# Optimization experiments

Measured on AMD Instinct MI355X. Metric: run time of the kernel, lower is better.

The kernel has to match this reference:

```python
import jax, jax.numpy as jnp
import numpy as np

N, E, G = 100000, 400000, 64
IN, H, C = 8, 4, 64
HD = H * C  # 256


def setup_inputs() -> dict:
    key = jax.random.key(0)
    ks = jax.random.split(key, 40)
    f = lambda k, shp, s=0.05: jax.random.normal(k, shp, jnp.float32) * s
    inp = {
        "x": jax.random.normal(ks[0], (N, IN), jnp.float32),
        "edge_attr": jax.random.normal(ks[1], (E, 1), jnp.float32),
        "src": jax.random.randint(ks[2], (E,), 0, N),
        "dst": jax.random.randint(ks[3], (E,), 0, N),
        "batch": jnp.sort(jax.random.randint(ks[4], (N,), 0, G)),
        # encoder Linear(8 -> 64)
        "W_enc": f(ks[5], (IN, C)), "b_enc": jnp.zeros((C,), jnp.float32),
        # GATv2 layer 1: in 64 -> H*C=256
        "g1_Wl": f(ks[6], (C, HD)), "g1_bl": jnp.zeros((HD,), jnp.float32),
        "g1_Wr": f(ks[7], (C, HD)), "g1_br": jnp.zeros((HD,), jnp.float32),
        "g1_We": f(ks[8], (1, HD)),
        "g1_att": f(ks[9], (H, C)),
        "g1_bias": jnp.zeros((HD,), jnp.float32),
        # GATv2 layer 2: in 256 -> 256
        "g2_Wl": f(ks[10], (HD, HD)), "g2_bl": jnp.zeros((HD,), jnp.float32),
        "g2_Wr": f(ks[11], (HD, HD)), "g2_br": jnp.zeros((HD,), jnp.float32),
        "g2_We": f(ks[12], (1, HD)),
        "g2_att": f(ks[13], (H, C)),
        "g2_bias": jnp.zeros((HD,), jnp.float32),
        # post MLP: 256 -> 128 -> LN -> relu -> 128 -> 64 -> relu, head 64 -> 1
        "W_p1": f(ks[14], (HD, 128)), "b_p1": jnp.zeros((128,), jnp.float32),
        "ln_g": jnp.ones((128,), jnp.float32), "ln_b": jnp.zeros((128,), jnp.float32),
        "W_p2": f(ks[15], (128, 64)), "b_p2": jnp.zeros((64,), jnp.float32),
        "W_head": f(ks[16], (64, 1)), "b_head": jnp.zeros((1,), jnp.float32),
    }
    return inp


def gatv2(x, src, dst, e_attr, Wl, bl, Wr, br, We, att, bias):
    """PyG GATv2Conv: score = att . LeakyReLU(xl[src] + xr[dst] + e), scatter-softmax over dst,
    out_i = sum_j alpha_ij * xl[j], concat heads, + bias."""
    n = x.shape[0]
    xl = (x @ Wl + bl).reshape(n, H, C)          # source-side transform
    xr = (x @ Wr + br).reshape(n, H, C)          # target-side transform
    ee = (e_attr @ We).reshape(-1, H, C)         # [E,H,C]
    s = jax.nn.leaky_relu(xl[src] + xr[dst] + ee, 0.2)
    logit = jnp.einsum('ehc,hc->eh', s, att)     # [E,H]
    # numerically-stable scatter softmax over edges sharing a target node
    m = jax.ops.segment_max(logit, dst, num_segments=n)
    m = jnp.where(jnp.isfinite(m), m, 0.0)
    ex = jnp.exp(logit - m[dst])
    den = jax.ops.segment_sum(ex, dst, num_segments=n)
    alpha = ex / (den[dst] + 1e-16)
    out = jax.ops.segment_sum(alpha[:, :, None] * xl[src], dst, num_segments=n)
    return out.reshape(n, HD) + bias


def reference(x, edge_attr, src, dst, batch,
              W_enc, b_enc,
              g1_Wl, g1_bl, g1_Wr, g1_br, g1_We, g1_att, g1_bias,
              g2_Wl, g2_bl, g2_Wr, g2_br, g2_We, g2_att, g2_bias,
              W_p1, b_p1, ln_g, ln_b, W_p2, b_p2, W_head, b_head):
    h = jax.nn.relu(x @ W_enc + b_enc)
    h = jax.nn.relu(gatv2(h, src, dst, edge_attr, g1_Wl, g1_bl, g1_Wr, g1_br, g1_We, g1_att, g1_bias))
    h = jax.nn.relu(gatv2(h, src, dst, edge_attr, g2_Wl, g2_bl, g2_Wr, g2_br, g2_We, g2_att, g2_bias))
    # global mean pool per graph
    sums = jax.ops.segment_sum(h, batch, num_segments=G)
    cnt = jax.ops.segment_sum(jnp.ones((h.shape[0],), h.dtype), batch, num_segments=G)
    p = sums / jnp.maximum(cnt, 1.0)[:, None]
    # post MLP (dropout is identity at inference)
    p = p @ W_p1 + b_p1
    mu = jnp.mean(p, axis=-1, keepdims=True)
    var = jnp.mean((p - mu) ** 2, axis=-1, keepdims=True)
    p = (p - mu) * jax.lax.rsqrt(var + 1e-5) * ln_g + ln_b
    p = jax.nn.relu(p)
    p = jax.nn.relu(p @ W_p2 + b_p2)
    return (p @ W_head + b_head)[:, 0]  # [G]
```

## Files before the change

### kernel.cpp

```cpp
#include <hip/hip_runtime.h>
#include <hip/hip_fp16.h>
#include <math.h>


#define HD 256
#define NHEAD 4
#define CH 64

typedef _Float16 half8 __attribute__((ext_vector_type(8)));
typedef _Float16 h2 __attribute__((ext_vector_type(2)));
typedef __attribute__((ext_vector_type(4))) float f32x4;

__device__ __forceinline__ h2 pack_h2(float a, float b) {
#if __has_builtin(__builtin_amdgcn_cvt_pkrtz)
    return __builtin_bit_cast(h2, __builtin_amdgcn_cvt_pkrtz(a, b));
#else
    return h2{(_Float16)a, (_Float16)b};
#endif
}

__device__ __forceinline__ void prep_one(const float* Wl, const float* Wr,
                                         ushort* frag, int K, int t) {
    int l = t & 63;
    int ct = (t >> 6) & 31;
    int ks = t >> 11;
    int n = l & 15, q = l >> 4;
    const float* W = (ct < 16) ? Wl : Wr;
    int col = (ct & 15) * 16 + n;
    ushort* phi = frag + (size_t)t * 8;
#pragma unroll
    for (int j = 0; j < 8; ++j) {
        int k = ks * 32 + q * 8 + j;
        float wv = W[(size_t)k * 256 + col];
        phi[j] = __half_as_ushort(__float2half(wv));
    }
}

__global__ void setup_kernel(int* __restrict__ zbase, int nzero,
                             const float* __restrict__ Wl1, const float* __restrict__ Wr1,
                             ushort* __restrict__ f1,
                             const float* __restrict__ Wl2, const float* __restrict__ Wr2,
                             ushort* __restrict__ f2) {
    int i = blockIdx.x * 256 + threadIdx.x;
    if (i < nzero) {
        zbase[i] = 0;
    } else {
        int gt = i - nzero;
        if (gt < 64 * 64) prep_one(Wl1, Wr1, f1, 64, gt);
        else if (gt < 64 * 64 + 256 * 64) prep_one(Wl2, Wr2, f2, 256, gt - 64 * 64);
    }
}

__global__ void deg_kernel(const int* __restrict__ dst, int* __restrict__ cnt, int E) {
    int e = blockIdx.x * 256 + threadIdx.x;
    if (e < E) atomicAdd(&cnt[dst[e]], 1);
}

__global__ void scan_block(const int* __restrict__ cnt, int* __restrict__ off,
                           int* __restrict__ bsum, int N) {
    __shared__ int s[256];
    int i = blockIdx.x * 256 + threadIdx.x;
    int v = (i < N) ? cnt[i] : 0;
    s[threadIdx.x] = v;
    __syncthreads();
    for (int d = 1; d < 256; d <<= 1) {
        int t = 0;
        if (threadIdx.x >= d) t = s[threadIdx.x - d];
        __syncthreads();
        s[threadIdx.x] += t;
        __syncthreads();
    }
    if (i < N) off[i + 1] = s[threadIdx.x];
    if (threadIdx.x == 255) bsum[blockIdx.x] = s[255];
    if (blockIdx.x == 0 && threadIdx.x == 0) off[0] = 0;
}

__global__ void scan_add2(int* __restrict__ off, const int* __restrict__ bsum, int N) {
    __shared__ int red[4];
    int b = blockIdx.x;
    int s = 0;
    for (int i = threadIdx.x; i < b; i += 256) s += bsum[i];
    for (int o = 32; o > 0; o >>= 1) s += __shfl_xor(s, o);
    if ((threadIdx.x & 63) == 0) red[threadIdx.x >> 6] = s;
    __syncthreads();
    int prefix = red[0] + red[1] + red[2] + red[3];
    int i = b * 256 + threadIdx.x;
    if (i < N) off[i + 1] += prefix;
}

__global__ void scatter_kernel(const int* __restrict__ dst, const int* __restrict__ src,
                               const float* __restrict__ eattr, const int* __restrict__ off,
                               int* __restrict__ cur, int2* __restrict__ edata, int E) {
    int e = blockIdx.x * 256 + threadIdx.x;
    if (e < E) {
        int d = dst[e];
        int p = atomicAdd(&cur[d], 1);
        edata[off[d] + p] = make_int2(src[e], __float_as_int(eattr[e]));
    }
}

template <int K, bool FUSE_ENC>
__global__ __launch_bounds__(512, 4) void gemm_mfma(
    const void* Av, const float* __restrict__ Wenc, const float* __restrict__ benc,
    const ushort* __restrict__ Bfrag,
    const float* __restrict__ bl, const float* __restrict__ br,
    ushort* __restrict__ outL, ushort* outR, int N) {
    constexpr int KS = K / 32;
    constexpr int C4 = K / 4;
    constexpr int LC4 = (K == 256) ? 6 : 4;
    constexpr int FRAG_SHORTS = KS * 4 * 64 * 8;
    constexpr int TB_STRIDE = 260;
    constexpr int SH_BYTES = (FRAG_SHORTS * 2 > 64 * TB_STRIDE * 2)
                                 ? FRAG_SHORTS * 2 : 64 * TB_STRIDE * 2;
    __shared__ __align__(16) char shraw[SH_BYTES];
    ushort* frag = (ushort*)shraw;
    ushort* tbuf = (ushort*)shraw;

    const int t = threadIdx.x;
    const int row0 = blockIdx.x * 64;
    const float* Ax = (const float*)Av;
    const ushort* Ahalf = (const ushort*)Av;

#pragma unroll
    for (int it = 0; it < (64 * C4) / 512; ++it) {
        int jj = it * 512 + t;
        int m = jj & 15;
        int c4 = (jj >> 4) & (C4 - 1);
        int rg = jj >> (4 + LC4);
        int row = row0 + rg * 16 + m;
        ushort4 sv = make_ushort4(0, 0, 0, 0);
        if constexpr (FUSE_ENC) {
            if (row < N) {
                float4 xa = *(const float4*)(Ax + (size_t)row * 8);
                float4 xb = *(const float4*)(Ax + (size_t)row * 8 + 4);
                float xrv[8] = {xa.x, xa.y, xa.z, xa.w, xb.x, xb.y, xb.z, xb.w};
                ushort o[4];
#pragma unroll
                for (int j = 0; j < 4; ++j) {
                    int c = c4 * 4 + j;
                    float a = benc[c];
#pragma unroll
                    for (int u = 0; u < 8; ++u) a = fmaf(xrv[u], Wenc[u * 64 + c], a);
                    o[j] = __half_as_ushort(__float2half(fmaxf(a, 0.f)));
                }
                sv = make_ushort4(o[0], o[1], o[2], o[3]);
            }
        } else {
            if (row < N) sv = *(const ushort4*)(Ahalf + (size_t)row * K + c4 * 4);
        }
        int c = c4 * 4;
        int ks = c >> 5, q = (c >> 3) & 3, jb = c & 7;
        int cell = (ks * 4 + rg) * 64 + m + 16 * q;
        *(ushort4*)(frag + cell * 8 + jb) = sv;
    }
    __syncthreads();

    const int w = t >> 6, l = t & 63;
    const int ct0 = w * 4;

    f32x4 acc[4][4];
#pragma unroll
    for (int rt = 0; rt < 4; ++rt)
#pragma unroll
        for (int c = 0; c < 4; ++c) acc[rt][c] = (f32x4){0.f, 0.f, 0.f, 0.f};

#pragma unroll
    for (int ks = 0; ks < KS; ++ks) {
        half8 a[4];
#pragma unroll
        for (int rt = 0; rt < 4; ++rt) {
            int cell = (ks * 4 + rt) * 64 + l;
            a[rt] = *(const half8*)(frag + cell * 8);
        }
#pragma unroll
        for (int c = 0; c < 4; ++c) {
            size_t e = ((size_t)(ks * 32 + ct0 + c) * 64 + l) * 8;
            half8 bh = *(const half8*)(Bfrag + e);
#pragma unroll
            for (int rt = 0; rt < 4; ++rt)
                acc[rt][c] = __builtin_amdgcn_mfma_f32_16x16x32_f16(a[rt], bh, acc[rt][c], 0, 0, 0);
        }
    }

    const int m = l & 15, q = l >> 4;
#pragma unroll
    for (int half = 0; half < 2; ++half) {
        __syncthreads();
        if ((w >> 2) == half) {
            const float* bias = half ? br : bl;
#pragma unroll
            for (int c = 0; c < 4; ++c) {
                int col = ((ct0 + c) & 15) * 16 + m;
                float bb = bias[col];
#pragma unroll
                for (int rt = 0; rt < 4; ++rt)
#pragma unroll
                    for (int r = 0; r < 4; ++r)
                        tbuf[(rt * 16 + q * 4 + r) * TB_STRIDE + col] =
                            __half_as_ushort(__float2half(acc[rt][c][r] + bb));
            }
        }
        __syncthreads();
        ushort* outp = half ? outR : outL;
#pragma unroll
        for (int it = 0; it < 4; ++it) {
            int jj = it * 512 + t;
            int row = jj >> 5;
            int ch = jj & 31;
            int grow = row0 + row;
            if (grow < N) {
                uint2 a0 = *(const uint2*)(tbuf + row * TB_STRIDE + ch * 8);
                uint2 a1 = *(const uint2*)(tbuf + row * TB_STRIDE + ch * 8 + 4);
                *(uint4*)(outp + (size_t)grow * 256 + ch * 8) =
                    make_uint4(a0.x, a0.y, a1.x, a1.y);
            }
        }
    }
}

__global__ __launch_bounds__(256) void gat_aggregate(
    const ushort* __restrict__ xl, const ushort* xr,
    const int* __restrict__ off, const int2* __restrict__ edata,
    const float* __restrict__ We, const float* __restrict__ att,
    const float* __restrict__ bias, ushort* out, int N) {
    int node = blockIdx.x * 4 + (threadIdx.x >> 6);
    if (node >= N) return;
    int lane = threadIdx.x & 63;
    int cbase = (lane >> 4) * 64 + (lane & 15) * 4;

    float4 wef = *(const float4*)(We + cbase);
    float4 atf = *(const float4*)(att + cbase);
    h2 we_lo = {(_Float16)wef.x, (_Float16)wef.y};
    h2 we_hi = {(_Float16)wef.z, (_Float16)wef.w};
    h2 at_lo = {(_Float16)atf.x, (_Float16)atf.y};
    h2 at_hi = {(_Float16)atf.z, (_Float16)atf.w};
    size_t nb = (size_t)node * HD;
    uint2 xru = *(const uint2*)(xr + nb + cbase);
    h2 xr_lo = __builtin_bit_cast(h2, xru.x);
    h2 xr_hi = __builtin_bit_cast(h2, xru.y);
    float4 b4 = *(const float4*)(bias + cbase);
    const h2 c02 = {(_Float16)0.2f, (_Float16)0.2f};
    const h2 z2 = {(_Float16)0.f, (_Float16)0.f};

    float l = 0.f;
    h2 acc_lo = z2, acc_hi = z2;

    int s0i = off[node], s1i = off[node + 1];
    int j[4];
    float ea[4];
#pragma unroll
    for (int u = 0; u < 4; ++u) {
        int tt = s0i + u;
        int2 ed = (tt < s1i) ? edata[tt] : make_int2(0, 0);
        j[u] = ed.x;
        ea[u] = __int_as_float(ed.y);
    }
    for (int t = s0i; t < s1i; t += 4) {
        int nE = s1i - t;
        if (nE > 4) nE = 4;
        int jc[4];
        float eac[4];
#pragma unroll
        for (int u = 0; u < 4; ++u) { jc[u] = j[u]; eac[u] = ea[u]; }
        h2 xlo[4], xhi[4];
#pragma unroll
        for (int u = 0; u < 4; ++u) {
            xlo[u] = z2; xhi[u] = z2;
            if (u < nE) {
                uint2 xu = *(const uint2*)(xl + (size_t)jc[u] * HD + cbase);
                xlo[u] = __builtin_bit_cast(h2, xu.x);
                xhi[u] = __builtin_bit_cast(h2, xu.y);
            }
        }
        if (t + 4 < s1i) {
#pragma unroll
            for (int u = 0; u < 4; ++u) {
                int tt = t + 4 + u;
                int2 ed = (tt < s1i) ? edata[tt] : make_int2(0, 0);
                j[u] = ed.x;
                ea[u] = __int_as_float(ed.y);
            }
        }
        float rr[4];
#pragma unroll
        for (int u = 0; u < 4; ++u) {
            _Float16 eh = (_Float16)eac[u];
            h2 e2 = {eh, eh};
            h2 s0 = e2 * we_lo + (xlo[u] + xr_lo);
            h2 s1 = e2 * we_hi + (xhi[u] + xr_hi);
            s0 = __builtin_elementwise_max(s0, z2) + __builtin_elementwise_min(s0, z2) * c02;
            s1 = __builtin_elementwise_max(s1, z2) + __builtin_elementwise_min(s1, z2) * c02;
            float v;
#if __has_builtin(__builtin_amdgcn_fdot2)
            v = __builtin_amdgcn_fdot2(__builtin_bit_cast(__fp16 __attribute__((ext_vector_type(2))), at_lo),
                                       __builtin_bit_cast(__fp16 __attribute__((ext_vector_type(2))), s0),
                                       0.f, false);
            v = __builtin_amdgcn_fdot2(__builtin_bit_cast(__fp16 __attribute__((ext_vector_type(2))), at_hi),
                                       __builtin_bit_cast(__fp16 __attribute__((ext_vector_type(2))), s1),
                                       v, false);
#else
            v = (float)at_lo.x * (float)s0.x + (float)at_lo.y * (float)s0.y
              + (float)at_hi.x * (float)s1.x + (float)at_hi.y * (float)s1.y;
#endif
            rr[u] = v;
        }
        h2 r01 = pack_h2(rr[0], rr[1]);
        h2 r23 = pack_h2(rr[2], rr[3]);
#pragma unroll
        for (int o = 1; o <= 8; o <<= 1) {
            int v01 = __shfl_xor(__builtin_bit_cast(int, r01), o);
            int v23 = __shfl_xor(__builtin_bit_cast(int, r23), o);
            r01 = r01 + __builtin_bit_cast(h2, v01);
            r23 = r23 + __builtin_bit_cast(h2, v23);
        }
        float r0 = (float)r01.x, r1 = (float)r01.y;
        float r2 = (float)r23.x, r3 = (float)r23.y;
        if (1 >= nE) r1 = -1e30f;
        if (2 >= nE) r2 = -1e30f;
        if (3 >= nE) r3 = -1e30f;
        float p0 = __expf(r0);
        float p1 = __expf(r1);
        float p2 = __expf(r2);
        float p3 = __expf(r3);
        l += (p0 + p1) + (p2 + p3);
        h2 ph0 = pack_h2(p0, p0);
        h2 ph1 = pack_h2(p1, p1);
        h2 ph2 = pack_h2(p2, p2);
        h2 ph3 = pack_h2(p3, p3);
        acc_lo = ph0 * xlo[0] + acc_lo;
        acc_hi = ph0 * xhi[0] + acc_hi;
        acc_lo = ph1 * xlo[1] + acc_lo;
        acc_hi = ph1 * xhi[1] + acc_hi;
        acc_lo = ph2 * xlo[2] + acc_lo;
        acc_hi = ph2 * xhi[2] + acc_hi;
        acc_lo = ph3 * xlo[3] + acc_lo;
        acc_hi = ph3 * xhi[3] + acc_hi;
    }
    float inv = 1.f / (l + 1e-16f);
    float ax = (float)acc_lo.x, ay = (float)acc_lo.y;
    float az = (float)acc_hi.x, aw = (float)acc_hi.y;
    ushort4 o;
    o.x = __half_as_ushort(__float2half(fmaxf(fmaf(ax, inv, b4.x), 0.f)));
    o.y = __half_as_ushort(__float2half(fmaxf(fmaf(ay, inv, b4.y), 0.f)));
    o.z = __half_as_ushort(__float2half(fmaxf(fmaf(az, inv, b4.z), 0.f)));
    o.w = __half_as_ushort(__float2half(fmaxf(fmaf(aw, inv, b4.w), 0.f)));
    *(ushort4*)(out + nb + cbase) = o;
}

__device__ __forceinline__ int lowerb(const int* b, int n, int v) {
    int lo = 0, hi = n;
    while (lo < hi) {
        int mid = (lo + hi) >> 1;
        if (b[mid] < v) lo = mid + 1; else hi = mid;
    }
    return lo;
}

__global__ void pool_kernel(const ushort* __restrict__ h, const int* __restrict__ batch,
                            float* __restrict__ pooled, float* __restrict__ gcnt, int N) {
    int g = blockIdx.x >> 3, part = blockIdx.x & 7;
    int start = lowerb(batch, N, g);
    int end = lowerb(batch, N, g + 1);
    int rows = end - start;
    int r0 = start + (int)((long long)rows * part / 8);
    int r1 = start + (int)((long long)rows * (part + 1) / 8);
    int c = threadIdx.x;
    float s = 0.f;
    for (int r = r0; r < r1; ++r)
        s += __half2float(__ushort_as_half(h[(size_t)r * HD + c]));
    atomicAdd(&pooled[g * HD + c], s);
    if (part == 0 && c == 0) gcnt[g] = (float)rows;
}

__global__ void mlp_kernel(const float* __restrict__ pooled, const float* __restrict__ gcnt,
                           const float* __restrict__ W_p1, const float* __restrict__ b_p1,
                           const float* __restrict__ ln_g, const float* __restrict__ ln_b,
                           const float* __restrict__ W_p2, const float* __restrict__ b_p2,
                           const float* __restrict__ W_head, const float* __restrict__ b_head,
                           float* __restrict__ out) {
    int g = blockIdx.x;
    int j = threadIdx.x;
    __shared__ float sh[128];
    __shared__ float red[2];

    float inv = 1.f / fmaxf(gcnt[g], 1.f);
    float v = b_p1[j];
    for (int k = 0; k < 256; ++k) v = fmaf(pooled[g * 256 + k] * inv, W_p1[k * 128 + j], v);

    float s = v;
    for (int o = 32; o > 0; o >>= 1) s += __shfl_xor(s, o);
    if ((j & 63) == 0) red[j >> 6] = s;
    __syncthreads();
    float mu = (red[0] + red[1]) * (1.f / 128.f);
    float d = v - mu;
    float s2 = d * d;
    for (int o = 32; o > 0; o >>= 1) s2 += __shfl_xor(s2, o);
    __syncthreads();
    if ((j & 63) == 0) red[j >> 6] = s2;
    __syncthreads();
    float var = (red[0] + red[1]) * (1.f / 128.f);

    float p = d * rsqrtf(var + 1e-5f) * ln_g[j] + ln_b[j];
    sh[j] = fmaxf(p, 0.f);
    __syncthreads();

    if (j < 64) {
        float q = b_p2[j];
        for (int k = 0; k < 128; ++k) q = fmaf(sh[k], W_p2[k * 64 + j], q);
        q = fmaxf(q, 0.f);
        float t = q * W_head[j];
        for (int o = 32; o > 0; o >>= 1) t += __shfl_xor(t, o);
        if (j == 0) out[g] = t + b_head[0];
    }
}

extern "C" void kernel_launch(void* const* d_in, const int* in_sizes, int n_in,
                              void* d_out, int out_size, void* d_ws, size_t ws_size,
                              hipStream_t stream) {
    const float* x      = (const float*)d_in[0];
    const float* eattr  = (const float*)d_in[1];
    const int*   src    = (const int*)d_in[2];
    const int*   dst    = (const int*)d_in[3];
    const int*   batch  = (const int*)d_in[4];
    const float* W_enc  = (const float*)d_in[5];
    const float* b_enc  = (const float*)d_in[6];
    const float* g1_Wl  = (const float*)d_in[7];
    const float* g1_bl  = (const float*)d_in[8];
    const float* g1_Wr  = (const float*)d_in[9];
    const float* g1_br  = (const float*)d_in[10];
    const float* g1_We  = (const float*)d_in[11];
    const float* g1_att = (const float*)d_in[12];
    const float* g1_bias= (const float*)d_in[13];
    const float* g2_Wl  = (const float*)d_in[14];
    const float* g2_bl  = (const float*)d_in[15];
    const float* g2_Wr  = (const float*)d_in[16];
    const float* g2_br  = (const float*)d_in[17];
    const float* g2_We  = (const float*)d_in[18];
    const float* g2_att = (const float*)d_in[19];
    const float* g2_bias= (const float*)d_in[20];
    const float* W_p1   = (const float*)d_in[21];
    const float* b_p1   = (const float*)d_in[22];
    const float* ln_g   = (const float*)d_in[23];
    const float* ln_b   = (const float*)d_in[24];
    const float* W_p2   = (const float*)d_in[25];
    const float* b_p2   = (const float*)d_in[26];
    const float* W_head = (const float*)d_in[27];
    const float* b_head = (const float*)d_in[28];

    const int N = in_sizes[0] / 8;
    const int E = in_sizes[2];

    char* p = (char*)d_ws;
    auto alloc = [&](size_t bytes) -> void* {
        void* r = (void*)p;
        p += (bytes + 255) & ~(size_t)255;
        return r;
    };
    ushort* bufA   = (ushort*)alloc((size_t)N * HD * 2);
    ushort* bufXL  = (ushort*)alloc((size_t)N * HD * 2);
    int*    cnt    = (int*)alloc((size_t)N * 4);
    int*    curp   = (int*)alloc((size_t)N * 4);
    float*  pooled = (float*)alloc(64 * HD * 4);
    char*   zend   = p;
    int*    off    = (int*)alloc((size_t)(N + 1) * 4);
    int2*   edata  = (int2*)alloc((size_t)E * 8);
    const int nb   = (N + 255) / 256;
    int*    bsum   = (int*)alloc((size_t)nb * 4);
    float*  gcnt   = (float*)alloc(64 * 4);
    ushort* wfrag1 = (ushort*)alloc((size_t)64 * 64 * 16 * 2);
    ushort* wfrag2 = (ushort*)alloc((size_t)256 * 64 * 16 * 2);

    const int nzero = (int)(((char*)zend - (char*)cnt) / 4);
    const int nsetup = nzero + 64 * 64 + 256 * 64;

    setup_kernel<<<(nsetup + 255) / 256, 256, 0, stream>>>(
        cnt, nzero, g1_Wl, g1_Wr, wfrag1, g2_Wl, g2_Wr, wfrag2);

    deg_kernel<<<(E + 255) / 256, 256, 0, stream>>>(dst, cnt, E);
    scan_block<<<nb, 256, 0, stream>>>(cnt, off, bsum, N);
    scan_add2<<<nb, 256, 0, stream>>>(off, bsum, N);
    scatter_kernel<<<(E + 255) / 256, 256, 0, stream>>>(dst, src, eattr, off, curp,
                                                        edata, E);

    const int gblocks = (N + 63) / 64;
    const int ablocks = (N + 3) / 4;

    gemm_mfma<64, true><<<gblocks, 512, 0, stream>>>(
        x, W_enc, b_enc, wfrag1, g1_bl, g1_br, bufXL, bufA, N);
    gat_aggregate<<<ablocks, 256, 0, stream>>>(
        bufXL, bufA, off, edata, g1_We, g1_att, g1_bias, bufA, N);

    gemm_mfma<256, false><<<gblocks, 512, 0, stream>>>(
        bufA, nullptr, nullptr, wfrag2, g2_bl, g2_br, bufXL, bufA, N);
    gat_aggregate<<<ablocks, 256, 0, stream>>>(
        bufXL, bufA, off, edata, g2_We, g2_att, g2_bias, bufA, N);

    pool_kernel<<<64 * 8, 256, 0, stream>>>(bufA, batch, pooled, gcnt, N);
    mlp_kernel<<<64, 128, 0, stream>>>(pooled, gcnt, W_p1, b_p1, ln_g, ln_b,
                                       W_p2, b_p2, W_head, b_head, (float*)d_out);
}
```

Baseline: 438.6 us.

## Process two nodes per wavefront in GAT aggregation with 16-byte gathers

```diff
diff --git a/kernel.cpp b/kernel.cpp
--- a/kernel.cpp
+++ b/kernel.cpp
@@ -16,6 +16,16 @@
     return __builtin_bit_cast(h2, __builtin_amdgcn_cvt_pkrtz(a, b));
 #else
     return h2{(_Float16)a, (_Float16)b};
+#endif
+}
+
+__device__ __forceinline__ float dot2f(h2 a, h2 b, float c) {
+#if __has_builtin(__builtin_amdgcn_fdot2)
+    typedef __fp16 fp16v2 __attribute__((ext_vector_type(2)));
+    return __builtin_amdgcn_fdot2(__builtin_bit_cast(fp16v2, a),
+                                  __builtin_bit_cast(fp16v2, b), c, false);
+#else
+    return c + (float)a.x * (float)b.x + (float)a.y * (float)b.y;
 #endif
 }
 
@@ -95,7 +105,7 @@
     if (e < E) {
         int d = dst[e];
         int p = atomicAdd(&cur[d], 1);
-        edata[off[d] + p] = make_int2(src[e], __float_as_int(eattr[e]));
+        edata[off[d] + p] = make_int2(src[e] << 9, __float_as_int(eattr[e]));
     }
 }
 
@@ -223,29 +233,45 @@
     const int* __restrict__ off, const int2* __restrict__ edata,
     const float* __restrict__ We, const float* __restrict__ att,
     const float* __restrict__ bias, ushort* out, int N) {
-    int node = blockIdx.x * 4 + (threadIdx.x >> 6);
-    if (node >= N) return;
-    int lane = threadIdx.x & 63;
-    int cbase = (lane >> 4) * 64 + (lane & 15) * 4;
-
-    float4 wef = *(const float4*)(We + cbase);
-    float4 atf = *(const float4*)(att + cbase);
-    h2 we_lo = {(_Float16)wef.x, (_Float16)wef.y};
-    h2 we_hi = {(_Float16)wef.z, (_Float16)wef.w};
-    h2 at_lo = {(_Float16)atf.x, (_Float16)atf.y};
-    h2 at_hi = {(_Float16)atf.z, (_Float16)atf.w};
-    size_t nb = (size_t)node * HD;
-    uint2 xru = *(const uint2*)(xr + nb + cbase);
-    h2 xr_lo = __builtin_bit_cast(h2, xru.x);
-    h2 xr_hi = __builtin_bit_cast(h2, xru.y);
-    float4 b4 = *(const float4*)(bias + cbase);
+    const int wid = blockIdx.x * 4 + (threadIdx.x >> 6);
+    if (wid * 2 >= N) return;
+    const int lane = threadIdx.x & 63;
+    const int l32 = lane & 31;
+    const int node = wid * 2 + (lane >> 5);
+    const int cbase = (l32 >> 3) * 64 + (l32 & 7) * 8;
+    const int cb2 = cbase * 2;
+
+    float4 wf0 = *(const float4*)(We + cbase);
+    float4 wf1 = *(const float4*)(We + cbase + 4);
+    float4 af0 = *(const float4*)(att + cbase);
+    float4 af1 = *(const float4*)(att + cbase + 4);
+    h2 we[4], at[4];
+    we[0] = pack_h2(wf0.x, wf0.y); we[1] = pack_h2(wf0.z, wf0.w);
+    we[2] = pack_h2(wf1.x, wf1.y); we[3] = pack_h2(wf1.z, wf1.w);
+    at[0] = pack_h2(af0.x, af0.y); at[1] = pack_h2(af0.z, af0.w);
+    at[2] = pack_h2(af1.x, af1.y); at[3] = pack_h2(af1.z, af1.w);
+
+    const h2 z2 = {(_Float16)0.f, (_Float16)0.f};
     const h2 c02 = {(_Float16)0.2f, (_Float16)0.2f};
-    const h2 z2 = {(_Float16)0.f, (_Float16)0.f};
-
+
+    const bool valid = node < N;
+    const size_t nb = (size_t)node * HD;
+    h2 xrv[4] = {z2, z2, z2, z2};
+    int s0i = 0, s1i = 0;
+    if (valid) {
+        uint4 xu = *(const uint4*)(xr + nb + cbase);
+        xrv[0] = __builtin_bit_cast(h2, xu.x);
+        xrv[1] = __builtin_bit_cast(h2, xu.y);
+        xrv[2] = __builtin_bit_cast(h2, xu.z);
+        xrv[3] = __builtin_bit_cast(h2, xu.w);
+        s0i = off[node];
+        s1i = off[node + 1];
+    }
+
+    const char* xlb = (const char*)xl;
     float l = 0.f;
-    h2 acc_lo = z2, acc_hi = z2;
-
-    int s0i = off[node], s1i = off[node + 1];
+    h2 acc[4] = {z2, z2, z2, z2};
+
     int j[4];
     float ea[4];
 #pragma unroll
@@ -255,59 +281,51 @@
         j[u] = ed.x;
         ea[u] = __int_as_float(ed.y);
     }
-    for (int t = s0i; t < s1i; t += 4) {
+    int t = s0i;
+    while (__any(t < s1i)) {
         int nE = s1i - t;
-        if (nE > 4) nE = 4;
+        nE = (nE > 4) ? 4 : nE;
         int jc[4];
         float eac[4];
 #pragma unroll
         for (int u = 0; u < 4; ++u) { jc[u] = j[u]; eac[u] = ea[u]; }
-        h2 xlo[4], xhi[4];
+        h2 xv[4][4];
 #pragma unroll
         for (int u = 0; u < 4; ++u) {
-            xlo[u] = z2; xhi[u] = z2;
+            xv[u][0] = z2; xv[u][1] = z2; xv[u][2] = z2; xv[u][3] = z2;
             if (u < nE) {
-                uint2 xu = *(const uint2*)(xl + (size_t)jc[u] * HD + cbase);
-                xlo[u] = __builtin_bit_cast(h2, xu.x);
-                xhi[u] = __builtin_bit_cast(h2, xu.y);
+                uint4 xu = *(const uint4*)(xlb + (unsigned)(jc[u] + cb2));
+                xv[u][0] = __builtin_bit_cast(h2, xu.x);
+                xv[u][1] = __builtin_bit_cast(h2, xu.y);
+                xv[u][2] = __builtin_bit_cast(h2, xu.z);
+                xv[u][3] = __builtin_bit_cast(h2, xu.w);
             }
         }
-        if (t + 4 < s1i) {
-#pragma unroll
-            for (int u = 0; u < 4; ++u) {
-                int tt = t + 4 + u;
-                int2 ed = (tt < s1i) ? edata[tt] : make_int2(0, 0);
-                j[u] = ed.x;
-                ea[u] = __int_as_float(ed.y);
-            }
+#pragma unroll
+        for (int u = 0; u < 4; ++u) {
+            int tt = t + 4 + u;
+            int2 ed = (tt < s1i) ? edata[tt] : make_int2(0, 0);
+            j[u] = ed.x;
+            ea[u] = __int_as_float(ed.y);
         }
         float rr[4];
 #pragma unroll
         for (int u = 0; u < 4; ++u) {
             _Float16 eh = (_Float16)eac[u];
             h2 e2 = {eh, eh};
-            h2 s0 = e2 * we_lo + (xlo[u] + xr_lo);
-            h2 s1 = e2 * we_hi + (xhi[u] + xr_hi);
-            s0 = __builtin_elementwise_max(s0, z2) + __builtin_elementwise_min(s0, z2) * c02;
-            s1 = __builtin_elementwise_max(s1, z2) + __builtin_elementwise_min(s1, z2) * c02;
-            float v;
-#if __has_builtin(__builtin_amdgcn_fdot2)
-            v = __builtin_amdgcn_fdot2(__builtin_bit_cast(__fp16 __attribute__((ext_vector_type(2))), at_lo),
-                                       __builtin_bit_cast(__fp16 __attribute__((ext_vector_type(2))), s0),
-                                       0.f, false);
-            v = __builtin_amdgcn_fdot2(__builtin_bit_cast(__fp16 __attribute__((ext_vector_type(2))), at_hi),
-                                       __builtin_bit_cast(__fp16 __attribute__((ext_vector_type(2))), s1),
-                                       v, false);
-#else
-            v = (float)at_lo.x * (float)s0.x + (float)at_lo.y * (float)s0.y
-              + (float)at_hi.x * (float)s1.x + (float)at_hi.y * (float)s1.y;
-#endif
+            float v = 0.f;
+#pragma unroll
+            for (int k = 0; k < 4; ++k) {
+                h2 s = e2 * we[k] + (xv[u][k] + xrv[k]);
+                s = __builtin_elementwise_max(s, z2) + __builtin_elementwise_min(s, z2) * c02;
+                v = dot2f(at[k], s, v);
+            }
             rr[u] = v;
         }
         h2 r01 = pack_h2(rr[0], rr[1]);
         h2 r23 = pack_h2(rr[2], rr[3]);
 #pragma unroll
-        for (int o = 1; o <= 8; o <<= 1) {
+        for (int o = 1; o <= 4; o <<= 1) {
             int v01 = __shfl_xor(__builtin_bit_cast(int, r01), o);
             int v23 = __shfl_xor(__builtin_bit_cast(int, r23), o);
             r01 = r01 + __builtin_bit_cast(h2, v01);
@@ -315,6 +333,7 @@
         }
         float r0 = (float)r01.x, r1 = (float)r01.y;
         float r2 = (float)r23.x, r3 = (float)r23.y;
+        if (0 >= nE) r0 = -1e30f;
         if (1 >= nE) r1 = -1e30f;
         if (2 >= nE) r2 = -1e30f;
         if (3 >= nE) r3 = -1e30f;
@@ -327,24 +346,37 @@
         h2 ph1 = pack_h2(p1, p1);
         h2 ph2 = pack_h2(p2, p2);
         h2 ph3 = pack_h2(p3, p3);
-        acc_lo = ph0 * xlo[0] + acc_lo;
-        acc_hi = ph0 * xhi[0] + acc_hi;
-        acc_lo = ph1 * xlo[1] + acc_lo;
-        acc_hi = ph1 * xhi[1] + acc_hi;
-        acc_lo = ph2 * xlo[2] + acc_lo;
-        acc_hi = ph2 * xhi[2] + acc_hi;
-        acc_lo = ph3 * xlo[3] + acc_lo;
-        acc_hi = ph3 * xhi[3] + acc_hi;
-    }
-    float inv = 1.f / (l + 1e-16f);
-    float ax = (float)acc_lo.x, ay = (float)acc_lo.y;
-    float az = (float)acc_hi.x, aw = (float)acc_hi.y;
-    ushort4 o;
-    o.x = __half_as_ushort(__float2half(fmaxf(fmaf(ax, inv, b4.x), 0.f)));
-    o.y = __half_as_ushort(__float2half(fmaxf(fmaf(ay, inv, b4.y), 0.f)));
-    o.z = __half_as_ushort(__float2half(fmaxf(fmaf(az, inv, b4.z), 0.f)));
-    o.w = __half_as_ushort(__float2half(fmaxf(fmaf(aw, inv, b4.w), 0.f)));
-    *(ushort4*)(out + nb + cbase) = o;
+#pragma unroll
+        for (int k = 0; k < 4; ++k) {
+            acc[k] = ph0 * xv[0][k] + acc[k];
+            acc[k] = ph1 * xv[1][k] + acc[k];
+            acc[k] = ph2 * xv[2][k] + acc[k];
+            acc[k] = ph3 * xv[3][k] + acc[k];
+        }
+        t += 4;
+    }
+    if (valid) {
+        float inv = 1.f / (l + 1e-16f);
+        float4 b0 = *(const float4*)(bias + cbase);
+        float4 b1 = *(const float4*)(bias + cbase + 4);
+        float q0 = fmaxf(fmaf((float)acc[0].x, inv, b0.x), 0.f);
+        float q1 = fmaxf(fmaf((float)acc[0].y, inv, b0.y), 0.f);
+        float q2 = fmaxf(fmaf((float)acc[1].x, inv, b0.z), 0.f);
+        float q3 = fmaxf(fmaf((float)acc[1].y, inv, b0.w), 0.f);
+        float q4 = fmaxf(fmaf((float)acc[2].x, inv, b1.x), 0.f);
+        float q5 = fmaxf(fmaf((float)acc[2].y, inv, b1.y), 0.f);
+        float q6 = fmaxf(fmaf((float)acc[3].x, inv, b1.z), 0.f);
+        float q7 = fmaxf(fmaf((float)acc[3].y, inv, b1.w), 0.f);
+        uint w0 = (uint)__half_as_ushort(__float2half(q0)) |
+                  ((uint)__half_as_ushort(__float2half(q1)) << 16);
+        uint w1 = (uint)__half_as_ushort(__float2half(q2)) |
+                  ((uint)__half_as_ushort(__float2half(q3)) << 16);
+        uint w2 = (uint)__half_as_ushort(__float2half(q4)) |
+                  ((uint)__half_as_ushort(__float2half(q5)) << 16);
+        uint w3 = (uint)__half_as_ushort(__float2half(q6)) |
+                  ((uint)__half_as_ushort(__float2half(q7)) << 16);
+        *(uint4*)(out + nb + cbase) = make_uint4(w0, w1, w2, w3);
+    }
 }
 
 __device__ __forceinline__ int lowerb(const int* b, int n, int v) {
@@ -483,7 +515,7 @@
                                                         edata, E);
 
     const int gblocks = (N + 63) / 64;
-    const int ablocks = (N + 3) / 4;
+    const int ablocks = (N + 7) / 8;
 
     gemm_mfma<64, true><<<gblocks, 512, 0, stream>>>(
         x, W_enc, b_enc, wfrag1, g1_bl, g1_br, bufXL, bufA, N);
```

Result: faster. 417.3 us (-4.9%).
